# Performance work log

Measured on AMD Instinct MI355X. Metric: run time of the kernel, lower is better.

## Reference

```python
import jax, jax.numpy as jnp
import numpy as np

B, S, D, H = 2, 2048, 1024, 16
HD = D // H


def setup_inputs() -> dict:
    key = jax.random.key(0)
    ks = jax.random.split(key, 9)
    x = jax.random.normal(ks[0], (B, S, D), dtype=jnp.float32)
    scale = 1.0 / np.sqrt(D)
    Wq = jax.random.normal(ks[1], (D, D), dtype=jnp.float32) * scale
    bq = jnp.zeros((D,), dtype=jnp.float32)
    Wk = jax.random.normal(ks[2], (D, D), dtype=jnp.float32) * scale
    bk = jnp.zeros((D,), dtype=jnp.float32)
    Wv = jax.random.normal(ks[3], (D, D), dtype=jnp.float32) * scale
    bv = jnp.zeros((D,), dtype=jnp.float32)
    Wo = jax.random.normal(ks[4], (D, D), dtype=jnp.float32) * scale
    bo = jnp.zeros((D,), dtype=jnp.float32)
    return {"x": x, "Wq": Wq, "bq": bq, "Wk": Wk, "bk": bk,
            "Wv": Wv, "bv": bv, "Wo": Wo, "bo": bo}


def reference(x, Wq, bq, Wk, bk, Wv, bv, Wo, bo):
    b, s, d = x.shape
    h, hd = H, HD
    # torch Linear: y = x @ W.T + b
    q = (x @ Wq.T + bq).reshape(b, s, h, hd).transpose(0, 2, 1, 3)  # (b,h,s,hd)
    k = (x @ Wk.T + bk).reshape(b, s, h, hd).transpose(0, 2, 1, 3)
    v = (x @ Wv.T + bv).reshape(b, s, h, hd).transpose(0, 2, 1, 3)
    scores = jnp.einsum('bhqd,bhkd->bhqk', q, k) / np.sqrt(hd)  # (b,h,s,s)
    # FAITHFUL to source: softmax over dim=1 (head axis), not the key axis.
    attn = jax.nn.softmax(scores, axis=1)
    # dropout is identity at inference
    out = jnp.einsum('bhqk,bhkd->bhqd', attn, v)  # (b,h,s,hd)
    out = out.transpose(0, 2, 1, 3).reshape(b, s, d)
    return out @ Wo.T + bo
```

## Files before the change

kernel.cpp:

```cpp
#include <hip/hip_runtime.h>
#include <hip/hip_bf16.h>
#include <cstdint>
#include <cstddef>


typedef __bf16 bf16x8 __attribute__((ext_vector_type(8)));
typedef __bf16 bf16x4 __attribute__((ext_vector_type(4)));
typedef _Float16 f16x2 __attribute__((ext_vector_type(2)));
typedef _Float16 f16x4 __attribute__((ext_vector_type(4)));
typedef _Float16 f16x8 __attribute__((ext_vector_type(8)));
typedef float floatx4 __attribute__((ext_vector_type(4)));

#define S_LEN 2048
#define DIM 1024
#define NH 16
#define HD 64
#define MTOT 4096
#define C_EXP 0.1803368801111244f

__device__ __forceinline__ float fast_exp2(float x) { return __builtin_amdgcn_exp2f(x); }

__device__ __forceinline__ f16x2 pk_cvt(float a, float b) {
    return __builtin_bit_cast(f16x2, __builtin_amdgcn_cvt_pkrtz(a, b));
}

__device__ __forceinline__ void g2l16(const void* g, void* l) {
    __builtin_amdgcn_global_load_lds(
        (const __attribute__((address_space(1))) void*)g,
        (__attribute__((address_space(3))) void*)l, 16, 0, 0);
}

__global__ void cast_all(const float* __restrict__ x,
                         const float* __restrict__ w0, const float* __restrict__ w1,
                         const float* __restrict__ w2, const float* __restrict__ w3,
                         __bf16* __restrict__ xb,
                         __bf16* __restrict__ o0, __bf16* __restrict__ o1,
                         __bf16* __restrict__ o2, _Float16* __restrict__ o3) {
    int bid = blockIdx.x;
    if (bid < 4096) {
        int i = (bid * 256 + threadIdx.x) * 4;
        float4 v = *(const float4*)&x[i];
        bf16x4 o;
        o.x = (__bf16)v.x; o.y = (__bf16)v.y; o.z = (__bf16)v.z; o.w = (__bf16)v.w;
        *(bf16x4*)&xb[i] = o;
        return;
    }
    bid -= 4096;
    int wi = bid >> 10;
    int i = ((bid & 1023) * 256 + threadIdx.x) * 4;
    if (wi == 3) {
        float4 v = *(const float4*)&w3[i];
        f16x4 o;
        o[0] = (_Float16)v.x; o[1] = (_Float16)v.y; o[2] = (_Float16)v.z; o[3] = (_Float16)v.w;
        *(f16x4*)&o3[i] = o;
        return;
    }
    const float* s = (wi == 0) ? w0 : (wi == 1) ? w1 : w2;
    __bf16* d = (wi == 0) ? o0 : (wi == 1) ? o1 : o2;
    float4 v = *(const float4*)&s[i];
    bf16x4 o;
    o.x = (__bf16)v.x; o.y = (__bf16)v.y; o.z = (__bf16)v.z; o.w = (__bf16)v.w;
    *(bf16x4*)&d[i] = o;
}

__global__ __launch_bounds__(256, 2) void qkv_gemm(const __bf16* __restrict__ A,
                                                   const __bf16* __restrict__ Wq,
                                                   const __bf16* __restrict__ Wk,
                                                   const __bf16* __restrict__ Wv,
                                                   const float* __restrict__ bq,
                                                   const float* __restrict__ bk,
                                                   const float* __restrict__ bv,
                                                   __bf16* __restrict__ Qo,
                                                   __bf16* __restrict__ Ko,
                                                   _Float16* __restrict__ Vt) {
    const int tng = blockIdx.x * 128, tm = blockIdx.y * 128;
    const int wsel = tng >> 10, tn = tng & 1023;
    const __bf16* W = (wsel == 0) ? Wq : (wsel == 1) ? Wk : Wv;
    const float* bias = (wsel == 0) ? bq : (wsel == 1) ? bk : bv;
    __shared__ __bf16 As[128 * 32];
    __shared__ __bf16 Bs[128 * 32];
    const int tid = threadIdx.x, wid = tid >> 6, lane = tid & 63;
    const int l15 = lane & 15, quad = lane >> 4;
    const int wm = (wid >> 1) * 64, wn = (wid & 1) * 64;
    floatx4 acc[4][4] = {};
    for (int k0 = 0; k0 < DIM; k0 += 32) {
        __syncthreads();
#pragma unroll
        for (int i = 0; i < 2; ++i) {
            int slot = i * 256 + tid;
            int r = slot >> 2, c8 = (slot & 3) * 8;
            g2l16(&A[(size_t)(tm + r) * DIM + k0 + c8], &As[slot * 8]);
            g2l16(&W[(size_t)(tn + r) * DIM + k0 + c8], &Bs[slot * 8]);
        }
        __syncthreads();
        bf16x8 af[4], bf[4];
#pragma unroll
        for (int t = 0; t < 4; ++t) {
            af[t] = *(const bf16x8*)&As[(wm + t * 16 + l15) * 32 + quad * 8];
            bf[t] = *(const bf16x8*)&Bs[(wn + t * 16 + l15) * 32 + quad * 8];
        }
#pragma unroll
        for (int im = 0; im < 4; ++im)
#pragma unroll
            for (int in = 0; in < 4; ++in)
                acc[im][in] = __builtin_amdgcn_mfma_f32_16x16x32_bf16(af[im], bf[in], acc[im][in], 0, 0, 0);
    }
    if (wsel < 2) {
        __bf16* O = wsel ? Ko : Qo;
#pragma unroll
        for (int im = 0; im < 4; ++im)
#pragma unroll
            for (int in = 0; in < 4; ++in)
#pragma unroll
                for (int r = 0; r < 4; ++r) {
                    int row = tm + wm + im * 16 + quad * 4 + r;
                    int col = tn + wn + in * 16 + l15;
                    O[(size_t)row * DIM + col] = (__bf16)(acc[im][in][r] + bias[col]);
                }
    } else {
#pragma unroll
        for (int im = 0; im < 4; ++im)
#pragma unroll
            for (int in = 0; in < 4; ++in) {
                int cv = tn + wn + in * 16 + l15;
                int row4 = tm + wm + im * 16 + quad * 4;
                float bv_ = bias[cv];
                f16x4 o;
#pragma unroll
                for (int r = 0; r < 4; ++r) o[r] = (_Float16)(acc[im][in][r] + bv_);
                *(f16x4*)&Vt[(size_t)cv * MTOT + row4] = o;
            }
    }
}

__global__ __launch_bounds__(512, 8) void den8(const __bf16* __restrict__ Q,
                                               const __bf16* __restrict__ Km,
                                               _Float16* __restrict__ rd) {
    const int kt = blockIdx.x * 64, qt = blockIdx.y * 128, b = blockIdx.z;
    __shared__ __bf16 Ks[2][2 * 2 * 64 * 32];
    const int tid = threadIdx.x, wid = tid >> 6, lane = tid & 63;
    const int l15 = lane & 15, quad = lane >> 4;
    const int wq = wid * 16;
    floatx4 dsum[4] = {};
    const size_t qrow = (size_t)(b * S_LEN + qt + wq + l15) * DIM;
    const size_t kbase = (size_t)(b * S_LEN + kt) * DIM;

#pragma unroll
    for (int i = 0; i < 2; ++i) {
        int slot = i * 512 + tid;
        int hs = slot >> 9, rem = slot & 511;
        int p = rem >> 8, rem2 = rem & 255;
        int r = rem2 >> 2, c8 = (rem2 & 3) * 8;
        g2l16(&Km[kbase + (size_t)r * DIM + hs * HD + p * 32 + c8], &Ks[0][slot * 8]);
    }
    for (int hh = 0; hh < 8; ++hh) {
        const int cur = hh & 1, nxt = cur ^ 1;
        __syncthreads();
        bf16x8 af[2][2];
#pragma unroll
        for (int hs = 0; hs < 2; ++hs) {
            af[hs][0] = *(const bf16x8*)&Q[qrow + (hh * 2 + hs) * HD + quad * 8];
            af[hs][1] = *(const bf16x8*)&Q[qrow + (hh * 2 + hs) * HD + 32 + quad * 8];
        }
        if (hh + 1 < 8) {
#pragma unroll
            for (int i = 0; i < 2; ++i) {
                int slot = i * 512 + tid;
                int hs = slot >> 9, rem = slot & 511;
                int p = rem >> 8, rem2 = rem & 255;
                int r = rem2 >> 2, c8 = (rem2 & 3) * 8;
                g2l16(&Km[kbase + (size_t)r * DIM + ((hh + 1) * 2 + hs) * HD + p * 32 + c8],
                      &Ks[nxt][slot * 8]);
            }
        }
#pragma unroll
        for (int hs = 0; hs < 2; ++hs) {
#pragma unroll
            for (int n = 0; n < 4; ++n) {
                bf16x8 b0 = *(const bf16x8*)&Ks[cur][hs * 4096 + (n * 16 + l15) * 32 + quad * 8];
                bf16x8 b1 = *(const bf16x8*)&Ks[cur][hs * 4096 + 2048 + (n * 16 + l15) * 32 + quad * 8];
                floatx4 acc = {};
                acc = __builtin_amdgcn_mfma_f32_16x16x32_bf16(af[hs][0], b0, acc, 0, 0, 0);
                acc = __builtin_amdgcn_mfma_f32_16x16x32_bf16(af[hs][1], b1, acc, 0, 0, 0);
                floatx4 sc = acc * C_EXP;
                floatx4 e;
#pragma unroll
                for (int r = 0; r < 4; ++r) e[r] = fast_exp2(sc[r]);
                dsum[n] += e;
            }
        }
    }
#pragma unroll
    for (int n = 0; n < 4; ++n)
#pragma unroll
        for (int r = 0; r < 4; ++r) {
            int q = qt + wq + quad * 4 + r;
            int k = kt + n * 16 + l15;
            rd[(size_t)(b * S_LEN + q) * S_LEN + k] = (_Float16)(1.0f / dsum[n][r]);
        }
}

__global__ __launch_bounds__(512, 8) void attn8(const __bf16* __restrict__ Q,
                                                const __bf16* __restrict__ Km,
                                                const _Float16* __restrict__ Vt,
                                                const _Float16* __restrict__ rd,
                                                _Float16* __restrict__ AO1,
                                                _Float16* __restrict__ AO2) {
    const int qt = (blockIdx.x >> 1) * 128, ks = blockIdx.x & 1;
    const int h = blockIdx.y, b = blockIdx.z;
    __shared__ __bf16 Ks[2][2 * 64 * 32];
    __shared__ _Float16 Vts[2][64 * 72];
    const int tid = threadIdx.x, wid = tid >> 6, lane = tid & 63;
    const int l15 = lane & 15, quad = lane >> 4;
    const int wq = wid * 16;
    const size_t qrow = (size_t)(b * S_LEN + qt + wq + l15) * DIM + h * HD;
    bf16x8 qf0 = *(const bf16x8*)&Q[qrow + quad * 8];
    bf16x8 qf1 = *(const bf16x8*)&Q[qrow + 32 + quad * 8];
    const _Float16* rdrow = &rd[(size_t)(b * S_LEN + qt + wq + l15) * S_LEN];
    floatx4 oacc[4] = {};
    const int kt0 = ks * (S_LEN / 2);
    const size_t kdim = (size_t)b * S_LEN * DIM;
    const int vr = tid >> 3, vc = (tid & 7) * 8;
    const int sp = tid >> 8, srem = tid & 255;
    const int sr = srem >> 2, sc8 = (srem & 3) * 8;

    {
        f16x8 vtmp = *(const f16x8*)&Vt[(size_t)(h * HD + vr) * MTOT + b * S_LEN + kt0 + vc];
        g2l16(&Km[kdim + (size_t)(kt0 + sr) * DIM + h * HD + sp * 32 + sc8], &Ks[0][tid * 8]);
        *(f16x8*)&Vts[0][vr * 72 + vc] = vtmp;
    }
    for (int it = 0; it < 16; ++it) {
        const int cur = it & 1, nxt = cur ^ 1;
        const int kt = kt0 + it * 64;
        __syncthreads();
        f16x4 rv[4];
#pragma unroll
        for (int mp = 0; mp < 4; ++mp)
            rv[mp] = *(const f16x4*)&rdrow[kt + mp * 16 + quad * 4];
        f16x8 vtmp;
        const bool has_next = (it + 1 < 16);
        if (has_next) {
            const int ktn = kt + 64;
            vtmp = *(const f16x8*)&Vt[(size_t)(h * HD + vr) * MTOT + b * S_LEN + ktn + vc];
            g2l16(&Km[kdim + (size_t)(ktn + sr) * DIM + h * HD + sp * 32 + sc8], &Ks[nxt][tid * 8]);
        }
#pragma unroll
        for (int mp = 0; mp < 4; ++mp) {
            bf16x8 kf0 = *(const bf16x8*)&Ks[cur][(mp * 16 + l15) * 32 + quad * 8];
            bf16x8 kf1 = *(const bf16x8*)&Ks[cur][2048 + (mp * 16 + l15) * 32 + quad * 8];
            floatx4 s = {};
            s = __builtin_amdgcn_mfma_f32_16x16x32_bf16(kf0, qf0, s, 0, 0, 0);
            s = __builtin_amdgcn_mfma_f32_16x16x32_bf16(kf1, qf1, s, 0, 0, 0);
            floatx4 sc = s * C_EXP;
            f16x2 p01 = pk_cvt(fast_exp2(sc[0]), fast_exp2(sc[1]));
            f16x2 p23 = pk_cvt(fast_exp2(sc[2]), fast_exp2(sc[3]));
            f16x4 pa = __builtin_shufflevector(p01, p23, 0, 1, 2, 3);
            pa = pa * rv[mp];
#pragma unroll
            for (int n = 0; n < 4; ++n) {
                f16x4 vb = *(const f16x4*)&Vts[cur][(n * 16 + l15) * 72 + mp * 16 + quad * 4];
                oacc[n] = __builtin_amdgcn_mfma_f32_16x16x16f16(pa, vb, oacc[n], 0, 0, 0);
            }
        }
        if (has_next) *(f16x8*)&Vts[nxt][vr * 72 + vc] = vtmp;
    }
    _Float16* AO = ks ? AO2 : AO1;
#pragma unroll
    for (int n = 0; n < 4; ++n)
#pragma unroll
        for (int r = 0; r < 4; ++r) {
            int row = qt + wq + quad * 4 + r;
            int col = h * HD + n * 16 + l15;
            AO[(size_t)(b * S_LEN + row) * DIM + col] = (_Float16)oacc[n][r];
        }
}

__global__ __launch_bounds__(256, 2) void gemm_out2(const _Float16* __restrict__ A1,
                                                    const _Float16* __restrict__ A2,
                                                    const _Float16* __restrict__ Bw,
                                                    const float* __restrict__ bias,
                                                    float* __restrict__ C) {
    const int tm = blockIdx.y * 128, tn = blockIdx.x * 64;
    __shared__ _Float16 As1[2 * 128 * 32];
    __shared__ _Float16 As2[2 * 128 * 32];
    __shared__ _Float16 Bs[2 * 64 * 32];
    const int tid = threadIdx.x, wid = tid >> 6, lane = tid & 63;
    const int l15 = lane & 15, quad = lane >> 4;
    const int wm = (wid >> 1) * 64, wn = (wid & 1) * 32;
    floatx4 acc[4][2] = {};
    for (int k0 = 0; k0 < DIM; k0 += 64) {
        __syncthreads();
#pragma unroll
        for (int i = 0; i < 4; ++i) {
            int slot = i * 256 + tid;
            int p = slot >> 9, rem = slot & 511;
            int r = rem >> 2, c8 = (rem & 3) * 8;
            size_t ga = (size_t)(tm + r) * DIM + k0 + p * 32 + c8;
            g2l16(&A1[ga], &As1[slot * 8]);
            g2l16(&A2[ga], &As2[slot * 8]);
        }
#pragma unroll
        for (int i = 0; i < 2; ++i) {
            int slot = i * 256 + tid;
            int p = slot >> 8, rem = slot & 255;
            int r = rem >> 2, c8 = (rem & 3) * 8;
            g2l16(&Bw[(size_t)(tn + r) * DIM + k0 + p * 32 + c8], &Bs[slot * 8]);
        }
        __syncthreads();
#pragma unroll
        for (int kc = 0; kc < 2; ++kc) {
            f16x8 af[4], bf[2];
#pragma unroll
            for (int t = 0; t < 4; ++t) {
                int off = kc * 4096 + (wm + t * 16 + l15) * 32 + quad * 8;
                f16x8 a1 = *(const f16x8*)&As1[off];
                f16x8 a2 = *(const f16x8*)&As2[off];
                af[t] = a1 + a2;
            }
#pragma unroll
            for (int t = 0; t < 2; ++t)
                bf[t] = *(const f16x8*)&Bs[kc * 2048 + (wn + t * 16 + l15) * 32 + quad * 8];
#pragma unroll
            for (int im = 0; im < 4; ++im)
#pragma unroll
                for (int in = 0; in < 2; ++in)
                    acc[im][in] = __builtin_amdgcn_mfma_f32_16x16x32_f16(af[im], bf[in], acc[im][in], 0, 0, 0);
        }
    }
#pragma unroll
    for (int im = 0; im < 4; ++im)
#pragma unroll
        for (int in = 0; in < 2; ++in)
#pragma unroll
            for (int r = 0; r < 4; ++r) {
                int row = tm + wm + im * 16 + quad * 4 + r;
                int col = tn + wn + in * 16 + l15;
                C[(size_t)row * DIM + col] = acc[im][in][r] + bias[col];
            }
}

extern "C" void kernel_launch(void* const* d_in, const int* in_sizes, int n_in,
                              void* d_out, int out_size, void* d_ws, size_t ws_size,
                              hipStream_t stream) {
    const float* x  = (const float*)d_in[0];
    const float* Wq = (const float*)d_in[1];
    const float* bq = (const float*)d_in[2];
    const float* Wk = (const float*)d_in[3];
    const float* bk = (const float*)d_in[4];
    const float* Wv = (const float*)d_in[5];
    const float* bv = (const float*)d_in[6];
    const float* Wo = (const float*)d_in[7];
    const float* bo = (const float*)d_in[8];
    float* out = (float*)d_out;

    char* ws = (char*)d_ws;
    const size_t MB = 1u << 20;
    __bf16*    xb  = (__bf16*)(ws);
    __bf16*    Wqb = (__bf16*)(ws + 8 * MB);
    __bf16*    Wkb = (__bf16*)(ws + 10 * MB);
    __bf16*    Wvb = (__bf16*)(ws + 12 * MB);
    _Float16*  Wof = (_Float16*)(ws + 14 * MB);
    __bf16*    Qb  = (__bf16*)(ws + 16 * MB);
    __bf16*    Kb  = (__bf16*)(ws + 24 * MB);
    _Float16*  VtH = (_Float16*)(ws + 32 * MB);
    _Float16*  rd  = (_Float16*)(ws + 40 * MB);
    _Float16*  AO1 = (_Float16*)(ws + 56 * MB);
    _Float16*  AO2 = (_Float16*)(ws + 64 * MB);

    cast_all<<<8192, 256, 0, stream>>>(x, Wq, Wk, Wv, Wo, xb, Wqb, Wkb, Wvb, Wof);

    qkv_gemm<<<dim3(24, 32), 256, 0, stream>>>(xb, Wqb, Wkb, Wvb, bq, bk, bv, Qb, Kb, VtH);

    den8<<<dim3(S_LEN / 64, S_LEN / 128, 2), 512, 0, stream>>>(Qb, Kb, rd);

    attn8<<<dim3((S_LEN / 128) * 2, NH, 2), 512, 0, stream>>>(Qb, Kb, VtH, rd, AO1, AO2);

    gemm_out2<<<dim3(DIM / 64, MTOT / 128), 256, 0, stream>>>(AO1, AO2, Wof, bo, out);
}
```

Before: 269.2 us.

## Double per-warp query rows in den/attn kernels and swizzle K shared tiles

Each warp in the denominator and attention kernels now handles 32 query rows instead of 16, so every K and V fragment read from shared memory feeds two MFMA tiles. This halves the block count and the LDS traffic per unit of compute. The K tile layout in shared memory is also XOR-style swizzled on load and read to reduce bank conflicts. In exchange, register pressure roughly doubles for accumulators, occupancy hints drop from 8 to 4, and there are fewer blocks to spread across CUs.

```diff
diff --git a/kernel.cpp b/kernel.cpp
--- a/kernel.cpp
+++ b/kernel.cpp
@@ -133,146 +133,174 @@
     }
 }
 
-__global__ __launch_bounds__(512, 8) void den8(const __bf16* __restrict__ Q,
+__global__ __launch_bounds__(512, 4) void den9(const __bf16* __restrict__ Q,
                                                const __bf16* __restrict__ Km,
                                                _Float16* __restrict__ rd) {
-    const int kt = blockIdx.x * 64, qt = blockIdx.y * 128, b = blockIdx.z;
+    const int kt = blockIdx.x * 64, qt = blockIdx.y * 256, b = blockIdx.z;
     __shared__ __bf16 Ks[2][2 * 2 * 64 * 32];
     const int tid = threadIdx.x, wid = tid >> 6, lane = tid & 63;
     const int l15 = lane & 15, quad = lane >> 4;
-    const int wq = wid * 16;
-    floatx4 dsum[4] = {};
-    const size_t qrow = (size_t)(b * S_LEN + qt + wq + l15) * DIM;
+    const int wq = wid * 32;
+    const int sw = (quad + l15 + (l15 >> 2)) & 3;
+    floatx4 dsum[2][4] = {};
+    const size_t qrow0 = (size_t)(b * S_LEN + qt + wq + l15) * DIM;
+    const size_t qrow1 = qrow0 + (size_t)16 * DIM;
     const size_t kbase = (size_t)(b * S_LEN + kt) * DIM;
-
+    int sidx[2]; size_t soff[2];
 #pragma unroll
     for (int i = 0; i < 2; ++i) {
         int slot = i * 512 + tid;
-        int hs = slot >> 9, rem = slot & 511;
-        int p = rem >> 8, rem2 = rem & 255;
-        int r = rem2 >> 2, c8 = (rem2 & 3) * 8;
-        g2l16(&Km[kbase + (size_t)r * DIM + hs * HD + p * 32 + c8], &Ks[0][slot * 8]);
-    }
+        int hs = slot >> 9, cj = slot & 511;
+        int p = cj >> 8, ci = cj & 255;
+        int st = ci >> 2, sj = ci & 3;
+        int sq = (sj - st - (st >> 2)) & 3;
+        sidx[i] = hs;
+        soff[i] = kbase + (size_t)st * DIM + p * 32 + sq * 8;
+    }
+#pragma unroll
+    for (int i = 0; i < 2; ++i)
+        g2l16(&Km[soff[i] + (0 * 2 + sidx[i]) * HD], &Ks[0][(i * 512 + tid) * 8]);
     for (int hh = 0; hh < 8; ++hh) {
         const int cur = hh & 1, nxt = cur ^ 1;
         __syncthreads();
-        bf16x8 af[2][2];
+        bf16x8 af[2][2][2];
 #pragma unroll
         for (int hs = 0; hs < 2; ++hs) {
-            af[hs][0] = *(const bf16x8*)&Q[qrow + (hh * 2 + hs) * HD + quad * 8];
-            af[hs][1] = *(const bf16x8*)&Q[qrow + (hh * 2 + hs) * HD + 32 + quad * 8];
+            int hoff = (hh * 2 + hs) * HD;
+            af[hs][0][0] = *(const bf16x8*)&Q[qrow0 + hoff + quad * 8];
+            af[hs][0][1] = *(const bf16x8*)&Q[qrow0 + hoff + 32 + quad * 8];
+            af[hs][1][0] = *(const bf16x8*)&Q[qrow1 + hoff + quad * 8];
+            af[hs][1][1] = *(const bf16x8*)&Q[qrow1 + hoff + 32 + quad * 8];
         }
         if (hh + 1 < 8) {
 #pragma unroll
-            for (int i = 0; i < 2; ++i) {
-                int slot = i * 512 + tid;
-                int hs = slot >> 9, rem = slot & 511;
-                int p = rem >> 8, rem2 = rem & 255;
-                int r = rem2 >> 2, c8 = (rem2 & 3) * 8;
-                g2l16(&Km[kbase + (size_t)r * DIM + ((hh + 1) * 2 + hs) * HD + p * 32 + c8],
-                      &Ks[nxt][slot * 8]);
-            }
+            for (int i = 0; i < 2; ++i)
+                g2l16(&Km[soff[i] + ((hh + 1) * 2 + sidx[i]) * HD], &Ks[nxt][(i * 512 + tid) * 8]);
         }
 #pragma unroll
         for (int hs = 0; hs < 2; ++hs) {
 #pragma unroll
             for (int n = 0; n < 4; ++n) {
-                bf16x8 b0 = *(const bf16x8*)&Ks[cur][hs * 4096 + (n * 16 + l15) * 32 + quad * 8];
-                bf16x8 b1 = *(const bf16x8*)&Ks[cur][hs * 4096 + 2048 + (n * 16 + l15) * 32 + quad * 8];
-                floatx4 acc = {};
-                acc = __builtin_amdgcn_mfma_f32_16x16x32_bf16(af[hs][0], b0, acc, 0, 0, 0);
-                acc = __builtin_amdgcn_mfma_f32_16x16x32_bf16(af[hs][1], b1, acc, 0, 0, 0);
-                floatx4 sc = acc * C_EXP;
-                floatx4 e;
-#pragma unroll
-                for (int r = 0; r < 4; ++r) e[r] = fast_exp2(sc[r]);
-                dsum[n] += e;
-            }
-        }
-    }
-#pragma unroll
-    for (int n = 0; n < 4; ++n)
-#pragma unroll
-        for (int r = 0; r < 4; ++r) {
-            int q = qt + wq + quad * 4 + r;
-            int k = kt + n * 16 + l15;
-            rd[(size_t)(b * S_LEN + q) * S_LEN + k] = (_Float16)(1.0f / dsum[n][r]);
-        }
-}
-
-__global__ __launch_bounds__(512, 8) void attn8(const __bf16* __restrict__ Q,
+                bf16x8 b0 = *(const bf16x8*)&Ks[cur][hs * 4096 + (n * 16 + l15) * 32 + sw * 8];
+                bf16x8 b1 = *(const bf16x8*)&Ks[cur][hs * 4096 + 2048 + (n * 16 + l15) * 32 + sw * 8];
+#pragma unroll
+                for (int sub = 0; sub < 2; ++sub) {
+                    floatx4 acc = {};
+                    acc = __builtin_amdgcn_mfma_f32_16x16x32_bf16(af[hs][sub][0], b0, acc, 0, 0, 0);
+                    acc = __builtin_amdgcn_mfma_f32_16x16x32_bf16(af[hs][sub][1], b1, acc, 0, 0, 0);
+                    floatx4 sc = acc * C_EXP;
+                    floatx4 e;
+#pragma unroll
+                    for (int r = 0; r < 4; ++r) e[r] = fast_exp2(sc[r]);
+                    dsum[sub][n] += e;
+                }
+            }
+        }
+    }
+#pragma unroll
+    for (int sub = 0; sub < 2; ++sub)
+#pragma unroll
+        for (int n = 0; n < 4; ++n)
+#pragma unroll
+            for (int r = 0; r < 4; ++r) {
+                int q = qt + wq + sub * 16 + quad * 4 + r;
+                int k = kt + n * 16 + l15;
+                rd[(size_t)(b * S_LEN + q) * S_LEN + k] = (_Float16)(1.0f / dsum[sub][n][r]);
+            }
+}
+
+__global__ __launch_bounds__(512, 4) void attn9(const __bf16* __restrict__ Q,
                                                 const __bf16* __restrict__ Km,
                                                 const _Float16* __restrict__ Vt,
                                                 const _Float16* __restrict__ rd,
                                                 _Float16* __restrict__ AO1,
                                                 _Float16* __restrict__ AO2) {
-    const int qt = (blockIdx.x >> 1) * 128, ks = blockIdx.x & 1;
+    const int qt = (blockIdx.x >> 1) * 256, ks = blockIdx.x & 1;
     const int h = blockIdx.y, b = blockIdx.z;
     __shared__ __bf16 Ks[2][2 * 64 * 32];
     __shared__ _Float16 Vts[2][64 * 72];
     const int tid = threadIdx.x, wid = tid >> 6, lane = tid & 63;
     const int l15 = lane & 15, quad = lane >> 4;
-    const int wq = wid * 16;
-    const size_t qrow = (size_t)(b * S_LEN + qt + wq + l15) * DIM + h * HD;
-    bf16x8 qf0 = *(const bf16x8*)&Q[qrow + quad * 8];
-    bf16x8 qf1 = *(const bf16x8*)&Q[qrow + 32 + quad * 8];
-    const _Float16* rdrow = &rd[(size_t)(b * S_LEN + qt + wq + l15) * S_LEN];
-    floatx4 oacc[4] = {};
+    const int wq = wid * 32;
+    const int sw = (quad + l15 + (l15 >> 2)) & 3;
+    const size_t qrow0 = (size_t)(b * S_LEN + qt + wq + l15) * DIM + h * HD;
+    const size_t qrow1 = qrow0 + (size_t)16 * DIM;
+    bf16x8 qf[2][2];
+    qf[0][0] = *(const bf16x8*)&Q[qrow0 + quad * 8];
+    qf[0][1] = *(const bf16x8*)&Q[qrow0 + 32 + quad * 8];
+    qf[1][0] = *(const bf16x8*)&Q[qrow1 + quad * 8];
+    qf[1][1] = *(const bf16x8*)&Q[qrow1 + 32 + quad * 8];
+    const _Float16* rdrow0 = &rd[(size_t)(b * S_LEN + qt + wq + l15) * S_LEN];
+    const _Float16* rdrow1 = rdrow0 + (size_t)16 * S_LEN;
+    floatx4 oacc[2][4] = {};
     const int kt0 = ks * (S_LEN / 2);
     const size_t kdim = (size_t)b * S_LEN * DIM;
     const int vr = tid >> 3, vc = (tid & 7) * 8;
-    const int sp = tid >> 8, srem = tid & 255;
-    const int sr = srem >> 2, sc8 = (srem & 3) * 8;
+    const int sp = tid >> 8, sci = tid & 255;
+    const int st = sci >> 2, sj = sci & 3;
+    const int sq = (sj - st - (st >> 2)) & 3;
+    const size_t ksrc = kdim + (size_t)st * DIM + h * HD + sp * 32 + sq * 8;
 
     {
         f16x8 vtmp = *(const f16x8*)&Vt[(size_t)(h * HD + vr) * MTOT + b * S_LEN + kt0 + vc];
-        g2l16(&Km[kdim + (size_t)(kt0 + sr) * DIM + h * HD + sp * 32 + sc8], &Ks[0][tid * 8]);
+        g2l16(&Km[ksrc + (size_t)kt0 * DIM], &Ks[0][tid * 8]);
         *(f16x8*)&Vts[0][vr * 72 + vc] = vtmp;
     }
     for (int it = 0; it < 16; ++it) {
         const int cur = it & 1, nxt = cur ^ 1;
         const int kt = kt0 + it * 64;
         __syncthreads();
-        f16x4 rv[4];
-#pragma unroll
-        for (int mp = 0; mp < 4; ++mp)
-            rv[mp] = *(const f16x4*)&rdrow[kt + mp * 16 + quad * 4];
+        f16x4 rv[2][4];
+#pragma unroll
+        for (int mp = 0; mp < 4; ++mp) {
+            rv[0][mp] = *(const f16x4*)&rdrow0[kt + mp * 16 + quad * 4];
+            rv[1][mp] = *(const f16x4*)&rdrow1[kt + mp * 16 + quad * 4];
+        }
         f16x8 vtmp;
         const bool has_next = (it + 1 < 16);
         if (has_next) {
             const int ktn = kt + 64;
             vtmp = *(const f16x8*)&Vt[(size_t)(h * HD + vr) * MTOT + b * S_LEN + ktn + vc];
-            g2l16(&Km[kdim + (size_t)(ktn + sr) * DIM + h * HD + sp * 32 + sc8], &Ks[nxt][tid * 8]);
+            g2l16(&Km[ksrc + (size_t)ktn * DIM], &Ks[nxt][tid * 8]);
         }
 #pragma unroll
         for (int mp = 0; mp < 4; ++mp) {
-            bf16x8 kf0 = *(const bf16x8*)&Ks[cur][(mp * 16 + l15) * 32 + quad * 8];
-            bf16x8 kf1 = *(const bf16x8*)&Ks[cur][2048 + (mp * 16 + l15) * 32 + quad * 8];
-            floatx4 s = {};
-            s = __builtin_amdgcn_mfma_f32_16x16x32_bf16(kf0, qf0, s, 0, 0, 0);
-            s = __builtin_amdgcn_mfma_f32_16x16x32_bf16(kf1, qf1, s, 0, 0, 0);
-            floatx4 sc = s * C_EXP;
-            f16x2 p01 = pk_cvt(fast_exp2(sc[0]), fast_exp2(sc[1]));
-            f16x2 p23 = pk_cvt(fast_exp2(sc[2]), fast_exp2(sc[3]));
-            f16x4 pa = __builtin_shufflevector(p01, p23, 0, 1, 2, 3);
-            pa = pa * rv[mp];
+            bf16x8 kf0 = *(const bf16x8*)&Ks[cur][(mp * 16 + l15) * 32 + sw * 8];
+            bf16x8 kf1 = *(const bf16x8*)&Ks[cur][2048 + (mp * 16 + l15) * 32 + sw * 8];
+            floatx4 s0 = {}, s1 = {};
+            s0 = __builtin_amdgcn_mfma_f32_16x16x32_bf16(kf0, qf[0][0], s0, 0, 0, 0);
+            s0 = __builtin_amdgcn_mfma_f32_16x16x32_bf16(kf1, qf[0][1], s0, 0, 0, 0);
+            s1 = __builtin_amdgcn_mfma_f32_16x16x32_bf16(kf0, qf[1][0], s1, 0, 0, 0);
+            s1 = __builtin_amdgcn_mfma_f32_16x16x32_bf16(kf1, qf[1][1], s1, 0, 0, 0);
+            floatx4 c0 = s0 * C_EXP, c1 = s1 * C_EXP;
+            f16x2 a01 = pk_cvt(fast_exp2(c0[0]), fast_exp2(c0[1]));
+            f16x2 a23 = pk_cvt(fast_exp2(c0[2]), fast_exp2(c0[3]));
+            f16x2 b01 = pk_cvt(fast_exp2(c1[0]), fast_exp2(c1[1]));
+            f16x2 b23 = pk_cvt(fast_exp2(c1[2]), fast_exp2(c1[3]));
+            f16x4 pa0 = __builtin_shufflevector(a01, a23, 0, 1, 2, 3);
+            f16x4 pa1 = __builtin_shufflevector(b01, b23, 0, 1, 2, 3);
+            pa0 = pa0 * rv[0][mp];
+            pa1 = pa1 * rv[1][mp];
 #pragma unroll
             for (int n = 0; n < 4; ++n) {
                 f16x4 vb = *(const f16x4*)&Vts[cur][(n * 16 + l15) * 72 + mp * 16 + quad * 4];
-                oacc[n] = __builtin_amdgcn_mfma_f32_16x16x16f16(pa, vb, oacc[n], 0, 0, 0);
+                oacc[0][n] = __builtin_amdgcn_mfma_f32_16x16x16f16(pa0, vb, oacc[0][n], 0, 0, 0);
+                oacc[1][n] = __builtin_amdgcn_mfma_f32_16x16x16f16(pa1, vb, oacc[1][n], 0, 0, 0);
             }
         }
         if (has_next) *(f16x8*)&Vts[nxt][vr * 72 + vc] = vtmp;
     }
     _Float16* AO = ks ? AO2 : AO1;
 #pragma unroll
-    for (int n = 0; n < 4; ++n)
-#pragma unroll
-        for (int r = 0; r < 4; ++r) {
-            int row = qt + wq + quad * 4 + r;
-            int col = h * HD + n * 16 + l15;
-            AO[(size_t)(b * S_LEN + row) * DIM + col] = (_Float16)oacc[n][r];
-        }
+    for (int sub = 0; sub < 2; ++sub)
+#pragma unroll
+        for (int n = 0; n < 4; ++n)
+#pragma unroll
+            for (int r = 0; r < 4; ++r) {
+                int row = qt + wq + sub * 16 + quad * 4 + r;
+                int col = h * HD + n * 16 + l15;
+                AO[(size_t)(b * S_LEN + row) * DIM + col] = (_Float16)oacc[sub][n][r];
+            }
 }
 
 __global__ __launch_bounds__(256, 2) void gemm_out2(const _Float16* __restrict__ A1,
@@ -371,9 +399,9 @@
 
     qkv_gemm<<<dim3(24, 32), 256, 0, stream>>>(xb, Wqb, Wkb, Wvb, bq, bk, bv, Qb, Kb, VtH);
 
-    den8<<<dim3(S_LEN / 64, S_LEN / 128, 2), 512, 0, stream>>>(Qb, Kb, rd);
-
-    attn8<<<dim3((S_LEN / 128) * 2, NH, 2), 512, 0, stream>>>(Qb, Kb, VtH, rd, AO1, AO2);
+    den9<<<dim3(S_LEN / 64, S_LEN / 256, 2), 512, 0, stream>>>(Qb, Kb, rd);
+
+    attn9<<<dim3((S_LEN / 256) * 2, NH, 2), 512, 0, stream>>>(Qb, Kb, VtH, rd, AO1, AO2);
 
     gemm_out2<<<dim3(DIM / 64, MTOT / 128), 256, 0, stream>>>(AO1, AO2, Wof, bo, out);
 }
```

Result: slower. 596.7 us (+121.6%).
